# Kernel tuning notes

Hardware: AMD Instinct MI355X
Metric: run time of the kernel (lower is better)

## Reference

```python
import math
import jax, jax.numpy as jnp
import numpy as np

H = 1024          # hidden size
NH = 16           # num attention heads
HD = H // NH      # head dim = 64
MAXPOS = 1024
HYP_W = 0.5


def setup_inputs() -> dict:
    key = jax.random.key(0)
    ks = jax.random.split(key, 9)
    B, S = 4, 1024
    scale = 1.0 / math.sqrt(H)
    return {
        "hidden_states": jax.random.normal(ks[0], (B, S, H), jnp.float32),
        "attention_mask": jnp.zeros((B, 1, 1, S), jnp.float32),
        "hyperbolic_attention_scores": jax.random.normal(ks[1], (B, S, S), jnp.float32),
        "Wq": jax.random.normal(ks[2], (H, H), jnp.float32) * scale,
        "bq": jnp.zeros((H,), jnp.float32),
        "Wk": jax.random.normal(ks[3], (H, H), jnp.float32) * scale,
        "bk": jnp.zeros((H,), jnp.float32),
        "Wv": jax.random.normal(ks[4], (H, H), jnp.float32) * scale,
        "bv": jnp.zeros((H,), jnp.float32),
        "dist_emb": jax.random.normal(ks[5], (2 * MAXPOS - 1, HD), jnp.float32) * 0.02,
    }


def reference(hidden_states, attention_mask, hyperbolic_attention_scores,
              Wq, bq, Wk, bk, Wv, bv, dist_emb):
    B, S, _ = hidden_states.shape

    def split_heads(x):  # [B,S,H] -> [B,NH,S,HD]
        return x.reshape(B, S, NH, HD).transpose(0, 2, 1, 3)

    q = split_heads(hidden_states @ Wq + bq)
    k = split_heads(hidden_states @ Wk + bk)
    v = split_heads(hidden_states @ Wv + bv)

    # raw scores [B,NH,Sq,Sk]
    scores = jnp.einsum("bhqd,bhkd->bhqk", q, k)

    # relative_key_query position bias
    distance = jnp.arange(S)[:, None] - jnp.arange(S)[None, :]  # [Sq,Sk]
    pe = dist_emb[distance + MAXPOS - 1]                        # [Sq,Sk,HD]
    scores = scores + jnp.einsum("bhld,lrd->bhlr", q, pe)
    scores = scores + jnp.einsum("bhrd,lrd->bhlr", k, pe)

    scores = scores / math.sqrt(HD)
    scores = scores + HYP_W * hyperbolic_attention_scores[:, None, :, :]
    scores = scores + attention_mask

    probs = jax.nn.softmax(scores, axis=-1)
    ctx = jnp.einsum("bhqk,bhkd->bhqd", probs, v)  # [B,NH,S,HD]
    ctx = ctx.transpose(0, 2, 1, 3).reshape(B, S, H)
    return ctx
```

## Files before the change

### kernel.cpp

```cpp
#include <hip/hip_runtime.h>
#include <math.h>

#define S_SEQ 1024
#define NHEAD 16
#define HDIM  64
#define BATCH 4

typedef __attribute__((ext_vector_type(8))) short bf16x8;
typedef __attribute__((ext_vector_type(4))) float f32x4;

__device__ __forceinline__ float bf2f(unsigned short h) {
    union { unsigned u; float f; } un; un.u = ((unsigned)h) << 16; return un.f;
}
__device__ __forceinline__ unsigned short f2bf(float x) {
    union { float f; unsigned u; } un; un.f = x;
    unsigned r = un.u + 0x7FFFu + ((un.u >> 16) & 1u);
    return (unsigned short)(r >> 16);
}

#define HS_F4 1048576
#define PE_F4 32752
__global__ __launch_bounds__(256) void conv_kernel(
    const float* __restrict__ hs, const float* __restrict__ de,
    unsigned short* __restrict__ hsb, unsigned short* __restrict__ peb)
{
    int i = blockIdx.x * 256 + threadIdx.x;
    if (i < HS_F4) {
        float4 v = ((const float4*)hs)[i];
        uint2 o;
        o.x = (unsigned)f2bf(v.x) | ((unsigned)f2bf(v.y) << 16);
        o.y = (unsigned)f2bf(v.z) | ((unsigned)f2bf(v.w) << 16);
        *(uint2*)(hsb + 4 * (size_t)i) = o;
    } else if (i < HS_F4 + PE_F4) {
        int j = i - HS_F4;
        float4 v = ((const float4*)de)[j];
        uint2 o;
        o.x = (unsigned)f2bf(v.x) | ((unsigned)f2bf(v.y) << 16);
        o.y = (unsigned)f2bf(v.z) | ((unsigned)f2bf(v.w) << 16);
        *(uint2*)(peb + 4 * (size_t)j) = o;
    }
}

__global__ __launch_bounds__(256) void wtrans_kernel(
    const float* __restrict__ Wq, const float* __restrict__ Wk,
    const float* __restrict__ Wv, unsigned short* __restrict__ wt)
{
    __shared__ float tl[64 * 67];
    const int which = blockIdx.z;
    const float* W = (which == 0) ? Wq : (which == 1) ? Wk : Wv;
    unsigned short* out = wt + (size_t)which * 1024 * 1024;
    const int k0 = blockIdx.x * 64, n0 = blockIdx.y * 64;
    const int t = threadIdx.x;

#pragma unroll
    for (int it = 0; it < 4; ++it) {
        int idx = t + it * 256;
        int kr = idx >> 4;
        int c4 = (idx & 15) << 2;
        float4 v = *(const float4*)(W + (size_t)(k0 + kr) * 1024 + n0 + c4);
        tl[kr * 67 + c4 + 0] = v.x; tl[kr * 67 + c4 + 1] = v.y;
        tl[kr * 67 + c4 + 2] = v.z; tl[kr * 67 + c4 + 3] = v.w;
    }
    __syncthreads();
#pragma unroll
    for (int it = 0; it < 2; ++it) {
        int idx = t + it * 256;
        int nr = idx >> 3;
        int k8 = (idx & 7) << 3;
        unsigned short r[8];
#pragma unroll
        for (int e = 0; e < 8; ++e) r[e] = f2bf(tl[(k8 + e) * 67 + nr]);
        uint4 o;
        o.x = (unsigned)r[0] | ((unsigned)r[1] << 16);
        o.y = (unsigned)r[2] | ((unsigned)r[3] << 16);
        o.z = (unsigned)r[4] | ((unsigned)r[5] << 16);
        o.w = (unsigned)r[6] | ((unsigned)r[7] << 16);
        *(uint4*)(out + (size_t)(n0 + nr) * 1024 + k0 + k8) = o;
    }
}

__global__ __launch_bounds__(256) void qkv_mfma_kernel(
    const unsigned short* __restrict__ hsb, const unsigned short* __restrict__ wt,
    const float* __restrict__ bq, const float* __restrict__ bk,
    const float* __restrict__ bv,
    unsigned short* __restrict__ qo, unsigned short* __restrict__ ko,
    unsigned short* __restrict__ vo)
{
    __shared__ unsigned short As[128 * 40];
    __shared__ unsigned short Bs[128 * 40];

    const int t = threadIdx.x;
    const int lane = t & 63, w = t >> 6;
    const int l16 = lane & 15, quad = lane >> 4;
    const int wm = w >> 1, wn = w & 1;
    const int n0 = blockIdx.x * 128, m0 = blockIdx.y * 128;
    const int which = blockIdx.z;
    const unsigned short* wts = wt + (size_t)which * 1024 * 1024;
    const float* bias = (which == 0) ? bq : (which == 1) ? bk : bv;
    unsigned short* out = (which == 0) ? qo : (which == 1) ? ko : vo;

    f32x4 acc[4][4];
#pragma unroll
    for (int i = 0; i < 4; ++i)
#pragma unroll
        for (int j = 0; j < 4; ++j) acc[i][j] = (f32x4){0.f, 0.f, 0.f, 0.f};

    for (int kk = 0; kk < 1024; kk += 32) {
#pragma unroll
        for (int it = 0; it < 2; ++it) {
            int idx = t + it * 256;
            int row = idx >> 2;
            int c8 = (idx & 3) << 3;
            *(uint4*)&As[row * 40 + c8] =
                *(const uint4*)(hsb + (size_t)(m0 + row) * 1024 + kk + c8);
            *(uint4*)&Bs[row * 40 + c8] =
                *(const uint4*)(wts + (size_t)(n0 + row) * 1024 + kk + c8);
        }
        __syncthreads();
        bf16x8 af[4], bf[4];
#pragma unroll
        for (int i = 0; i < 4; ++i)
            af[i] = *(bf16x8*)&As[(64 * wm + 16 * i + l16) * 40 + quad * 8];
#pragma unroll
        for (int j = 0; j < 4; ++j)
            bf[j] = *(bf16x8*)&Bs[(64 * wn + 16 * j + l16) * 40 + quad * 8];
#pragma unroll
        for (int i = 0; i < 4; ++i)
#pragma unroll
            for (int j = 0; j < 4; ++j)
                acc[i][j] = __builtin_amdgcn_mfma_f32_16x16x32_bf16(
                    af[i], bf[j], acc[i][j], 0, 0, 0);
        __syncthreads();
    }

#pragma unroll
    for (int j = 0; j < 4; ++j) {
        int n = n0 + 64 * wn + 16 * j + l16;
        float bvv = bias[n];
        int hh = n >> 6, hd = n & 63;
#pragma unroll
        for (int i = 0; i < 4; ++i)
#pragma unroll
            for (int r = 0; r < 4; ++r) {
                int m = m0 + 64 * wm + 16 * i + quad * 4 + r;
                int bb = m >> 10, s = m & 1023;
                out[((size_t)(bb * NHEAD + hh) * S_SEQ + s) * HDIM + hd] =
                    f2bf(acc[i][j][r] + bvv);
            }
    }
}

__global__ __launch_bounds__(256, 2) void attn_mfma_kernel(
    const unsigned short* __restrict__ qw, const unsigned short* __restrict__ kw,
    const unsigned short* __restrict__ vw, const unsigned short* __restrict__ peb,
    const float* __restrict__ hyp, const float* __restrict__ mask,
    float* __restrict__ out)
{
    __shared__ unsigned short ks[64 * 72];
    __shared__ unsigned short vsb[64 * 72];
    __shared__ unsigned short pes[128 * 72];
    __shared__ unsigned short QDs[128 * 68];
    __shared__ unsigned short KDs[128 * 68];

    const int t = threadIdx.x;
    const int lane = t & 63, w = t >> 6;
    const int l16 = lane & 15, quad = lane >> 4;
    const int l0 = blockIdx.x * 64;
    const int h = blockIdx.y, b = blockIdx.z;

    const unsigned short* qb = qw + ((size_t)(b * NHEAD + h) * S_SEQ + l0) * HDIM;
    const unsigned short* kb = kw + (size_t)(b * NHEAD + h) * S_SEQ * HDIM;
    const unsigned short* vb = vw + (size_t)(b * NHEAD + h) * S_SEQ * HDIM;
    const float* hypb  = hyp + (size_t)b * S_SEQ * S_SEQ;
    const float* maskb = mask + b * S_SEQ;

    bf16x8 qf[2];
    qf[0] = *(const bf16x8*)(qb + (16 * w + l16) * 64 + quad * 8);
    qf[1] = *(const bf16x8*)(qb + (16 * w + l16) * 64 + 32 + quad * 8);

    if (t < 8) *(uint4*)&pes[127 * 72 + t * 8] = (uint4){0, 0, 0, 0};

    f32x4 accO[4];
#pragma unroll
    for (int j = 0; j < 4; ++j) accO[j] = (f32x4){0.f, 0.f, 0.f, 0.f};
    float m_run[4], lsum[4];
#pragma unroll
    for (int i = 0; i < 4; ++i) { m_run[i] = -INFINITY; lsum[i] = 0.f; }

    for (int kt = 0; kt < 16; ++kt) {
        const int r0 = kt * 64;
        __syncthreads();
#pragma unroll
        for (int it = 0; it < 2; ++it) {
            int idx = t + it * 256;
            int row = idx >> 3, c8 = (idx & 7) << 3;
            *(uint4*)&ks[row * 72 + c8] =
                *(const uint4*)(kb + (size_t)(r0 + row) * 64 + c8);
        }
#pragma unroll
        for (int it = 0; it < 2; ++it) {
            int idx = t + it * 256;
            int vr = idx >> 3, d8 = (idx & 7) << 3;
            uint4 raw = *(const uint4*)(vb + (size_t)(r0 + vr) * 64 + d8);
            const unsigned short* pv = (const unsigned short*)&raw;
            int chunk = (((vr >> 3) ^ (d8 >> 3)) << 3) | (vr & 7);
#pragma unroll
            for (int e = 0; e < 8; ++e) vsb[(d8 + e) * 72 + chunk] = pv[e];
        }
        {
            const size_t pbase = (size_t)(l0 - r0 + 960) * 64;
            for (int idx = t; idx < 1016; idx += 256) {
                int row = idx >> 3, c8 = (idx & 7) << 3;
                *(uint4*)&pes[row * 72 + c8] = *(const uint4*)(peb + pbase + row * 64 + c8);
            }
        }
        __syncthreads();

        bf16x8 kfA[2];
        kfA[0] = *(bf16x8*)&ks[(16 * w + l16) * 72 + quad * 8];
        kfA[1] = *(bf16x8*)&ks[(16 * w + l16) * 72 + 32 + quad * 8];
        f32x4 accS[4];
#pragma unroll
        for (int j = 0; j < 4; ++j) {
            bf16x8 b0 = *(bf16x8*)&ks[(16 * j + l16) * 72 + quad * 8];
            bf16x8 b1 = *(bf16x8*)&ks[(16 * j + l16) * 72 + 32 + quad * 8];
            f32x4 a = (f32x4){0.f, 0.f, 0.f, 0.f};
            a = __builtin_amdgcn_mfma_f32_16x16x32_bf16(qf[0], b0, a, 0, 0, 0);
            a = __builtin_amdgcn_mfma_f32_16x16x32_bf16(qf[1], b1, a, 0, 0, 0);
            accS[j] = a;
        }
#pragma unroll
        for (int jd = 0; jd < 8; ++jd) {
            bf16x8 p0 = *(bf16x8*)&pes[(16 * jd + l16) * 72 + quad * 8];
            bf16x8 p1 = *(bf16x8*)&pes[(16 * jd + l16) * 72 + 32 + quad * 8];
            f32x4 aq = (f32x4){0.f, 0.f, 0.f, 0.f};
            f32x4 ak = (f32x4){0.f, 0.f, 0.f, 0.f};
            aq = __builtin_amdgcn_mfma_f32_16x16x32_bf16(qf[0], p0, aq, 0, 0, 0);
            aq = __builtin_amdgcn_mfma_f32_16x16x32_bf16(qf[1], p1, aq, 0, 0, 0);
            ak = __builtin_amdgcn_mfma_f32_16x16x32_bf16(kfA[0], p0, ak, 0, 0, 0);
            ak = __builtin_amdgcn_mfma_f32_16x16x32_bf16(kfA[1], p1, ak, 0, 0, 0);
            uint2 oq, okk;
            oq.x  = (unsigned)f2bf(aq[0]) | ((unsigned)f2bf(aq[1]) << 16);
            oq.y  = (unsigned)f2bf(aq[2]) | ((unsigned)f2bf(aq[3]) << 16);
            okk.x = (unsigned)f2bf(ak[0]) | ((unsigned)f2bf(ak[1]) << 16);
            okk.y = (unsigned)f2bf(ak[2]) | ((unsigned)f2bf(ak[3]) << 16);
            *(uint2*)&QDs[(16 * jd + l16) * 68 + 16 * w + 4 * quad] = oq;
            *(uint2*)&KDs[(16 * jd + l16) * 68 + 16 * w + 4 * quad] = okk;
        }
        __syncthreads();

        float sc[4][4];
#pragma unroll
        for (int j = 0; j < 4; ++j) {
            int r_loc = 16 * j + l16;
            float mv = maskb[r0 + r_loc];
#pragma unroll
            for (int i = 0; i < 4; ++i) {
                int ll = 16 * w + 4 * quad + i;
                int di = ll - r_loc + 63;
                float qd = bf2f(QDs[di * 68 + ll]);
                float kd = bf2f(KDs[di * 68 + r_loc]);
                float hv = hypb[(size_t)(l0 + ll) * S_SEQ + r0 + r_loc];
                sc[i][j] = (accS[j][i] + qd + kd) * 0.125f + 0.5f * hv + mv;
            }
        }
        float al[4];
#pragma unroll
        for (int i = 0; i < 4; ++i) {
            float mx = fmaxf(fmaxf(sc[i][0], sc[i][1]), fmaxf(sc[i][2], sc[i][3]));
#pragma unroll
            for (int off = 1; off < 16; off <<= 1)
                mx = fmaxf(mx, __shfl_xor(mx, off));
            float m_new = fmaxf(m_run[i], mx);
            al[i] = __expf(m_run[i] - m_new);
            float rs = 0.f;
#pragma unroll
            for (int j = 0; j < 4; ++j) {
                float p = __expf(sc[i][j] - m_new);
                sc[i][j] = p;
                rs += p;
            }
#pragma unroll
            for (int off = 1; off < 16; off <<= 1)
                rs += __shfl_xor(rs, off);
            lsum[i] = lsum[i] * al[i] + rs;
            m_run[i] = m_new;
        }
#pragma unroll
        for (int i = 0; i < 4; ++i)
#pragma unroll
            for (int j = 0; j < 4; ++j)
                pes[(16 * w + 4 * quad + i) * 72 + 16 * j + l16] = f2bf(sc[i][j]);
        __syncthreads();

        bf16x8 pf[2];
        pf[0] = *(bf16x8*)&pes[(16 * w + l16) * 72 + quad * 8];
        pf[1] = *(bf16x8*)&pes[(16 * w + l16) * 72 + 32 + quad * 8];
#pragma unroll
        for (int j = 0; j < 4; ++j) {
            int d = 16 * j + l16;
            int c0 = ((quad ^ (d >> 3)) << 3);
            int c1 = (((4 + quad) ^ (d >> 3)) << 3);
            bf16x8 v0 = *(bf16x8*)&vsb[d * 72 + c0];
            bf16x8 v1 = *(bf16x8*)&vsb[d * 72 + c1];
            f32x4 o = accO[j];
#pragma unroll
            for (int r = 0; r < 4; ++r) o[r] *= al[r];
            o = __builtin_amdgcn_mfma_f32_16x16x32_bf16(pf[0], v0, o, 0, 0, 0);
            o = __builtin_amdgcn_mfma_f32_16x16x32_bf16(pf[1], v1, o, 0, 0, 0);
            accO[j] = o;
        }
    }

#pragma unroll
    for (int j = 0; j < 4; ++j)
#pragma unroll
        for (int i = 0; i < 4; ++i) {
            int ll = 16 * w + 4 * quad + i;
            out[((size_t)b * S_SEQ + l0 + ll) * 1024 + h * 64 + 16 * j + l16] =
                accO[j][i] / lsum[i];
        }
}

extern "C" void kernel_launch(void* const* d_in, const int* in_sizes, int n_in,
                              void* d_out, int out_size, void* d_ws, size_t ws_size,
                              hipStream_t stream) {
    const float* hs   = (const float*)d_in[0];
    const float* mask = (const float*)d_in[1];
    const float* hyp  = (const float*)d_in[2];
    const float* Wq   = (const float*)d_in[3];
    const float* bq   = (const float*)d_in[4];
    const float* Wk   = (const float*)d_in[5];
    const float* bk   = (const float*)d_in[6];
    const float* Wv   = (const float*)d_in[7];
    const float* bv   = (const float*)d_in[8];
    const float* de   = (const float*)d_in[9];

    char* ws = (char*)d_ws;
    unsigned short* qw  = (unsigned short*)(ws);
    unsigned short* kw  = (unsigned short*)(ws + (8u << 20));
    unsigned short* vw  = (unsigned short*)(ws + (16u << 20));
    unsigned short* hsb = (unsigned short*)(ws + (24u << 20));
    unsigned short* wt  = (unsigned short*)(ws + (32u << 20));
    unsigned short* peb = (unsigned short*)(ws + (38u << 20));

    conv_kernel<<<dim3((HS_F4 + PE_F4 + 255) / 256), 256, 0, stream>>>(hs, de, hsb, peb);
    wtrans_kernel<<<dim3(16, 16, 3), 256, 0, stream>>>(Wq, Wk, Wv, wt);
    qkv_mfma_kernel<<<dim3(8, 32, 3), 256, 0, stream>>>(hsb, wt, bq, bk, bv, qw, kw, vw);
    attn_mfma_kernel<<<dim3(16, NHEAD, BATCH), 256, 0, stream>>>(
        qw, kw, vw, peb, hyp, mask, (float*)d_out);
}
```

Baseline: 312.7 us.

## Rework attention with ring-buffered position embeddings, pre-transposed V, and async-LDS QKV loads

The attention kernel now uses 32-key tiles and keeps position-embedding rows in a 96-slot ring buffer, so each tile loads only 32 new rows and computes only the new query-distance products instead of recomputing all of them. The QKV GEMM writes V pre-transposed, which removes the scalar transpose into shared memory inside the attention loop. The GEMM also uses K=64 tiles with XOR-swizzled LDS and global_load_lds direct loads. Occupancy hints rise to 3 blocks per CU. The cost is twice as many tile iterations and barriers, plus more complex slot indexing that could be wrong.

```diff
diff --git a/kernel.cpp b/kernel.cpp
--- a/kernel.cpp
+++ b/kernel.cpp
@@ -16,6 +16,14 @@
     union { float f; unsigned u; } un; un.f = x;
     unsigned r = un.u + 0x7FFFu + ((un.u >> 16) & 1u);
     return (unsigned short)(r >> 16);
+}
+__device__ __forceinline__ unsigned pack2bf(float a, float b) {
+    return (unsigned)f2bf(a) | ((unsigned)f2bf(b) << 16);
+}
+__device__ __forceinline__ void glds16(const unsigned short* g, unsigned short* l) {
+    __builtin_amdgcn_global_load_lds(
+        (const __attribute__((address_space(1))) void*)g,
+        (__attribute__((address_space(3))) void*)l, 16, 0, 0);
 }
 
 #define HS_F4 1048576
@@ -28,15 +36,15 @@
     if (i < HS_F4) {
         float4 v = ((const float4*)hs)[i];
         uint2 o;
-        o.x = (unsigned)f2bf(v.x) | ((unsigned)f2bf(v.y) << 16);
-        o.y = (unsigned)f2bf(v.z) | ((unsigned)f2bf(v.w) << 16);
+        o.x = pack2bf(v.x, v.y);
+        o.y = pack2bf(v.z, v.w);
         *(uint2*)(hsb + 4 * (size_t)i) = o;
     } else if (i < HS_F4 + PE_F4) {
         int j = i - HS_F4;
         float4 v = ((const float4*)de)[j];
         uint2 o;
-        o.x = (unsigned)f2bf(v.x) | ((unsigned)f2bf(v.y) << 16);
-        o.y = (unsigned)f2bf(v.z) | ((unsigned)f2bf(v.w) << 16);
+        o.x = pack2bf(v.x, v.y);
+        o.y = pack2bf(v.z, v.w);
         *(uint2*)(peb + 4 * (size_t)j) = o;
     }
 }
@@ -79,25 +87,25 @@
     }
 }
 
-__global__ __launch_bounds__(256) void qkv_mfma_kernel(
+__global__ __launch_bounds__(256, 3) void qkv_mfma_kernel(
     const unsigned short* __restrict__ hsb, const unsigned short* __restrict__ wt,
     const float* __restrict__ bq, const float* __restrict__ bk,
     const float* __restrict__ bv,
     unsigned short* __restrict__ qo, unsigned short* __restrict__ ko,
     unsigned short* __restrict__ vo)
 {
-    __shared__ unsigned short As[128 * 40];
-    __shared__ unsigned short Bs[128 * 40];
+    __shared__ unsigned short As[128 * 64];
+    __shared__ unsigned short Bs[128 * 64];
 
     const int t = threadIdx.x;
     const int lane = t & 63, w = t >> 6;
     const int l16 = lane & 15, quad = lane >> 4;
     const int wm = w >> 1, wn = w & 1;
+    const int lrow = lane >> 3, cs = lane & 7;
     const int n0 = blockIdx.x * 128, m0 = blockIdx.y * 128;
     const int which = blockIdx.z;
     const unsigned short* wts = wt + (size_t)which * 1024 * 1024;
     const float* bias = (which == 0) ? bq : (which == 1) ? bk : bv;
-    unsigned short* out = (which == 0) ? qo : (which == 1) ? ko : vo;
 
     f32x4 acc[4][4];
 #pragma unroll
@@ -105,31 +113,42 @@
 #pragma unroll
         for (int j = 0; j < 4; ++j) acc[i][j] = (f32x4){0.f, 0.f, 0.f, 0.f};
 
-    for (int kk = 0; kk < 1024; kk += 32) {
-#pragma unroll
-        for (int it = 0; it < 2; ++it) {
-            int idx = t + it * 256;
-            int row = idx >> 2;
-            int c8 = (idx & 3) << 3;
-            *(uint4*)&As[row * 40 + c8] =
-                *(const uint4*)(hsb + (size_t)(m0 + row) * 1024 + kk + c8);
-            *(uint4*)&Bs[row * 40 + c8] =
-                *(const uint4*)(wts + (size_t)(n0 + row) * 1024 + kk + c8);
-        }
-        __syncthreads();
-        bf16x8 af[4], bf[4];
+    for (int kk = 0; kk < 1024; kk += 64) {
+#pragma unroll
+        for (int it = 0; it < 4; ++it) {
+            int mrow = 32 * w + 8 * it + lrow;
+            int kch = cs ^ (mrow & 7);
+            glds16(hsb + (size_t)(m0 + mrow) * 1024 + kk + kch * 8,
+                   &As[(32 * w + 8 * it) * 64]);
+            glds16(wts + (size_t)(n0 + mrow) * 1024 + kk + kch * 8,
+                   &Bs[(32 * w + 8 * it) * 64]);
+        }
+        __syncthreads();
+
+        bf16x8 af[4][2], bf[4][2];
+#pragma unroll
+        for (int i = 0; i < 4; ++i) {
+            int am = 64 * wm + 16 * i + l16;
+            int base = am * 64;
+            af[i][0] = *(bf16x8*)&As[base + ((quad ^ (am & 7)) << 3)];
+            af[i][1] = *(bf16x8*)&As[base + (((quad + 4) ^ (am & 7)) << 3)];
+        }
+#pragma unroll
+        for (int j = 0; j < 4; ++j) {
+            int bn = 64 * wn + 16 * j + l16;
+            int base = bn * 64;
+            bf[j][0] = *(bf16x8*)&Bs[base + ((quad ^ (bn & 7)) << 3)];
+            bf[j][1] = *(bf16x8*)&Bs[base + (((quad + 4) ^ (bn & 7)) << 3)];
+        }
 #pragma unroll
         for (int i = 0; i < 4; ++i)
-            af[i] = *(bf16x8*)&As[(64 * wm + 16 * i + l16) * 40 + quad * 8];
-#pragma unroll
-        for (int j = 0; j < 4; ++j)
-            bf[j] = *(bf16x8*)&Bs[(64 * wn + 16 * j + l16) * 40 + quad * 8];
-#pragma unroll
-        for (int i = 0; i < 4; ++i)
-#pragma unroll
-            for (int j = 0; j < 4; ++j)
+#pragma unroll
+            for (int j = 0; j < 4; ++j) {
                 acc[i][j] = __builtin_amdgcn_mfma_f32_16x16x32_bf16(
-                    af[i], bf[j], acc[i][j], 0, 0, 0);
+                    af[i][0], bf[j][0], acc[i][j], 0, 0, 0);
+                acc[i][j] = __builtin_amdgcn_mfma_f32_16x16x32_bf16(
+                    af[i][1], bf[j][1], acc[i][j], 0, 0, 0);
+            }
         __syncthreads();
     }
 
@@ -139,28 +158,37 @@
         float bvv = bias[n];
         int hh = n >> 6, hd = n & 63;
 #pragma unroll
-        for (int i = 0; i < 4; ++i)
-#pragma unroll
-            for (int r = 0; r < 4; ++r) {
-                int m = m0 + 64 * wm + 16 * i + quad * 4 + r;
-                int bb = m >> 10, s = m & 1023;
-                out[((size_t)(bb * NHEAD + hh) * S_SEQ + s) * HDIM + hd] =
-                    f2bf(acc[i][j][r] + bvv);
+        for (int i = 0; i < 4; ++i) {
+            int mb = m0 + 64 * wm + 16 * i + 4 * quad;
+            int bb = mb >> 10, s = mb & 1023;
+            if (which == 2) {
+                uint2 o;
+                o.x = pack2bf(acc[i][j][0] + bvv, acc[i][j][1] + bvv);
+                o.y = pack2bf(acc[i][j][2] + bvv, acc[i][j][3] + bvv);
+                *(uint2*)(vo + ((size_t)(bb * NHEAD + hh) * HDIM + hd) * S_SEQ + s) = o;
+            } else {
+                unsigned short* out = (which == 0) ? qo : ko;
+#pragma unroll
+                for (int r = 0; r < 4; ++r)
+                    out[((size_t)(bb * NHEAD + hh) * S_SEQ + s + r) * HDIM + hd] =
+                        f2bf(acc[i][j][r] + bvv);
             }
-    }
-}
-
-__global__ __launch_bounds__(256, 2) void attn_mfma_kernel(
+        }
+    }
+}
+
+__global__ __launch_bounds__(256, 3) void attn_mfma_kernel(
     const unsigned short* __restrict__ qw, const unsigned short* __restrict__ kw,
-    const unsigned short* __restrict__ vw, const unsigned short* __restrict__ peb,
+    const unsigned short* __restrict__ vtw, const unsigned short* __restrict__ peb,
     const float* __restrict__ hyp, const float* __restrict__ mask,
     float* __restrict__ out)
 {
-    __shared__ unsigned short ks[64 * 72];
-    __shared__ unsigned short vsb[64 * 72];
-    __shared__ unsigned short pes[128 * 72];
-    __shared__ unsigned short QDs[128 * 68];
-    __shared__ unsigned short KDs[128 * 68];
+    __shared__ unsigned short ks[32 * 72];
+    __shared__ unsigned short vT[64 * 40];
+    __shared__ unsigned short pes[96 * 72];
+    __shared__ unsigned short QDs[96 * 66];
+    __shared__ unsigned short KDs[96 * 38];
+    __shared__ unsigned short ps[64 * 40];
 
     const int t = threadIdx.x;
     const int lane = t & 63, w = t >> 6;
@@ -170,15 +198,37 @@
 
     const unsigned short* qb = qw + ((size_t)(b * NHEAD + h) * S_SEQ + l0) * HDIM;
     const unsigned short* kb = kw + (size_t)(b * NHEAD + h) * S_SEQ * HDIM;
-    const unsigned short* vb = vw + (size_t)(b * NHEAD + h) * S_SEQ * HDIM;
-    const float* hypb  = hyp + (size_t)b * S_SEQ * S_SEQ;
+    const unsigned short* vtb = vtw + (size_t)(b * NHEAD + h) * HDIM * S_SEQ;
+    const float* hypb = hyp + (size_t)b * S_SEQ * S_SEQ;
     const float* maskb = mask + b * S_SEQ;
 
-    bf16x8 qf[2];
-    qf[0] = *(const bf16x8*)(qb + (16 * w + l16) * 64 + quad * 8);
-    qf[1] = *(const bf16x8*)(qb + (16 * w + l16) * 64 + 32 + quad * 8);
-
-    if (t < 8) *(uint4*)&pes[127 * 72 + t * 8] = (uint4){0, 0, 0, 0};
+    const bf16x8 qf0 = *(const bf16x8*)(qb + (16 * w + l16) * 64 + quad * 8);
+    const bf16x8 qf1 = *(const bf16x8*)(qb + (16 * w + l16) * 64 + 32 + quad * 8);
+
+    const int pb0 = l0 + 992;
+
+#pragma unroll
+    for (int it = 0; it < 2; ++it) {
+        int idx = t + it * 256;
+        int row = idx >> 3, c8 = (idx & 7) << 3;
+        int ar = pb0 + 32 + row;
+        int slot = ar % 96;
+        int src = ar > 2046 ? 2046 : ar;
+        *(uint4*)&pes[slot * 72 + c8] = *(const uint4*)(peb + (size_t)src * 64 + c8);
+    }
+    __syncthreads();
+#pragma unroll
+    for (int jd = 0; jd < 4; ++jd) {
+        int slot = (pb0 + 32 + 16 * jd + l16) % 96;
+        bf16x8 p0 = *(bf16x8*)&pes[slot * 72 + quad * 8];
+        bf16x8 p1 = *(bf16x8*)&pes[slot * 72 + 32 + quad * 8];
+        f32x4 aq = (f32x4){0.f, 0.f, 0.f, 0.f};
+        aq = __builtin_amdgcn_mfma_f32_16x16x32_bf16(qf0, p0, aq, 0, 0, 0);
+        aq = __builtin_amdgcn_mfma_f32_16x16x32_bf16(qf1, p1, aq, 0, 0, 0);
+        int ad = slot * 66 + 16 * w + 4 * quad;
+        *(unsigned*)&QDs[ad] = pack2bf(aq[0], aq[1]);
+        *(unsigned*)&QDs[ad + 2] = pack2bf(aq[2], aq[3]);
+    }
 
     f32x4 accO[4];
 #pragma unroll
@@ -187,99 +237,92 @@
 #pragma unroll
     for (int i = 0; i < 4; ++i) { m_run[i] = -INFINITY; lsum[i] = 0.f; }
 
-    for (int kt = 0; kt < 16; ++kt) {
-        const int r0 = kt * 64;
-        __syncthreads();
-#pragma unroll
-        for (int it = 0; it < 2; ++it) {
-            int idx = t + it * 256;
-            int row = idx >> 3, c8 = (idx & 7) << 3;
+    int sb = pb0 % 96;
+
+    for (int kt = 0; kt < 32; ++kt) {
+        const int r0 = 32 * kt;
+        const int pb = pb0 - r0;
+
+        {
+            int row = t >> 3, c8 = (t & 7) << 3;
             *(uint4*)&ks[row * 72 + c8] =
                 *(const uint4*)(kb + (size_t)(r0 + row) * 64 + c8);
-        }
-#pragma unroll
-        for (int it = 0; it < 2; ++it) {
-            int idx = t + it * 256;
-            int vr = idx >> 3, d8 = (idx & 7) << 3;
-            uint4 raw = *(const uint4*)(vb + (size_t)(r0 + vr) * 64 + d8);
-            const unsigned short* pv = (const unsigned short*)&raw;
-            int chunk = (((vr >> 3) ^ (d8 >> 3)) << 3) | (vr & 7);
-#pragma unroll
-            for (int e = 0; e < 8; ++e) vsb[(d8 + e) * 72 + chunk] = pv[e];
-        }
-        {
-            const size_t pbase = (size_t)(l0 - r0 + 960) * 64;
-            for (int idx = t; idx < 1016; idx += 256) {
-                int row = idx >> 3, c8 = (idx & 7) << 3;
-                *(uint4*)&pes[row * 72 + c8] = *(const uint4*)(peb + pbase + row * 64 + c8);
-            }
-        }
-        __syncthreads();
-
-        bf16x8 kfA[2];
-        kfA[0] = *(bf16x8*)&ks[(16 * w + l16) * 72 + quad * 8];
-        kfA[1] = *(bf16x8*)&ks[(16 * w + l16) * 72 + 32 + quad * 8];
-        f32x4 accS[4];
-#pragma unroll
-        for (int j = 0; j < 4; ++j) {
+            int d = t >> 2, rc = (t & 3) << 3;
+            *(uint4*)&vT[d * 40 + rc] =
+                *(const uint4*)(vtb + (size_t)d * 1024 + r0 + rc);
+            int slot = sb + row; if (slot >= 96) slot -= 96;
+            *(uint4*)&pes[slot * 72 + c8] =
+                *(const uint4*)(peb + (size_t)(pb + row) * 64 + c8);
+        }
+        __syncthreads();
+
+        bf16x8 kfA0 = *(bf16x8*)&ks[(16 * (w & 1) + l16) * 72 + quad * 8];
+        bf16x8 kfA1 = *(bf16x8*)&ks[(16 * (w & 1) + l16) * 72 + 32 + quad * 8];
+        f32x4 accS[2];
+#pragma unroll
+        for (int j = 0; j < 2; ++j) {
             bf16x8 b0 = *(bf16x8*)&ks[(16 * j + l16) * 72 + quad * 8];
             bf16x8 b1 = *(bf16x8*)&ks[(16 * j + l16) * 72 + 32 + quad * 8];
             f32x4 a = (f32x4){0.f, 0.f, 0.f, 0.f};
-            a = __builtin_amdgcn_mfma_f32_16x16x32_bf16(qf[0], b0, a, 0, 0, 0);
-            a = __builtin_amdgcn_mfma_f32_16x16x32_bf16(qf[1], b1, a, 0, 0, 0);
+            a = __builtin_amdgcn_mfma_f32_16x16x32_bf16(qf0, b0, a, 0, 0, 0);
+            a = __builtin_amdgcn_mfma_f32_16x16x32_bf16(qf1, b1, a, 0, 0, 0);
             accS[j] = a;
         }
 #pragma unroll
-        for (int jd = 0; jd < 8; ++jd) {
-            bf16x8 p0 = *(bf16x8*)&pes[(16 * jd + l16) * 72 + quad * 8];
-            bf16x8 p1 = *(bf16x8*)&pes[(16 * jd + l16) * 72 + 32 + quad * 8];
+        for (int jd = 0; jd < 2; ++jd) {
+            int slot = sb + 16 * jd + l16; if (slot >= 96) slot -= 96;
+            bf16x8 p0 = *(bf16x8*)&pes[slot * 72 + quad * 8];
+            bf16x8 p1 = *(bf16x8*)&pes[slot * 72 + 32 + quad * 8];
             f32x4 aq = (f32x4){0.f, 0.f, 0.f, 0.f};
+            aq = __builtin_amdgcn_mfma_f32_16x16x32_bf16(qf0, p0, aq, 0, 0, 0);
+            aq = __builtin_amdgcn_mfma_f32_16x16x32_bf16(qf1, p1, aq, 0, 0, 0);
+            int ad = slot * 66 + 16 * w + 4 * quad;
+            *(unsigned*)&QDs[ad] = pack2bf(aq[0], aq[1]);
+            *(unsigned*)&QDs[ad + 2] = pack2bf(aq[2], aq[3]);
+        }
+#pragma unroll
+        for (int jk = 0; jk < 3; ++jk) {
+            int dd = 48 * (w >> 1) + 16 * jk + l16;
+            int slot = sb + dd; if (slot >= 96) slot -= 96;
+            bf16x8 p0 = *(bf16x8*)&pes[slot * 72 + quad * 8];
+            bf16x8 p1 = *(bf16x8*)&pes[slot * 72 + 32 + quad * 8];
             f32x4 ak = (f32x4){0.f, 0.f, 0.f, 0.f};
-            aq = __builtin_amdgcn_mfma_f32_16x16x32_bf16(qf[0], p0, aq, 0, 0, 0);
-            aq = __builtin_amdgcn_mfma_f32_16x16x32_bf16(qf[1], p1, aq, 0, 0, 0);
-            ak = __builtin_amdgcn_mfma_f32_16x16x32_bf16(kfA[0], p0, ak, 0, 0, 0);
-            ak = __builtin_amdgcn_mfma_f32_16x16x32_bf16(kfA[1], p1, ak, 0, 0, 0);
-            uint2 oq, okk;
-            oq.x  = (unsigned)f2bf(aq[0]) | ((unsigned)f2bf(aq[1]) << 16);
-            oq.y  = (unsigned)f2bf(aq[2]) | ((unsigned)f2bf(aq[3]) << 16);
-            okk.x = (unsigned)f2bf(ak[0]) | ((unsigned)f2bf(ak[1]) << 16);
-            okk.y = (unsigned)f2bf(ak[2]) | ((unsigned)f2bf(ak[3]) << 16);
-            *(uint2*)&QDs[(16 * jd + l16) * 68 + 16 * w + 4 * quad] = oq;
-            *(uint2*)&KDs[(16 * jd + l16) * 68 + 16 * w + 4 * quad] = okk;
-        }
-        __syncthreads();
-
-        float sc[4][4];
-#pragma unroll
-        for (int j = 0; j < 4; ++j) {
+            ak = __builtin_amdgcn_mfma_f32_16x16x32_bf16(kfA0, p0, ak, 0, 0, 0);
+            ak = __builtin_amdgcn_mfma_f32_16x16x32_bf16(kfA1, p1, ak, 0, 0, 0);
+            int ad = dd * 38 + 16 * (w & 1) + 4 * quad;
+            *(unsigned*)&KDs[ad] = pack2bf(ak[0], ak[1]);
+            *(unsigned*)&KDs[ad + 2] = pack2bf(ak[2], ak[3]);
+        }
+        __syncthreads();
+
+        float sc[4][2], al[4];
+#pragma unroll
+        for (int j = 0; j < 2; ++j) {
             int r_loc = 16 * j + l16;
             float mv = maskb[r0 + r_loc];
 #pragma unroll
             for (int i = 0; i < 4; ++i) {
                 int ll = 16 * w + 4 * quad + i;
-                int di = ll - r_loc + 63;
-                float qd = bf2f(QDs[di * 68 + ll]);
-                float kd = bf2f(KDs[di * 68 + r_loc]);
-                float hv = hypb[(size_t)(l0 + ll) * S_SEQ + r0 + r_loc];
+                int di = ll - r_loc + 31;
+                int sl = sb + di; if (sl >= 96) sl -= 96;
+                float qd = bf2f(QDs[sl * 66 + ll]);
+                float kd = bf2f(KDs[di * 38 + r_loc]);
+                float hv = hypb[(size_t)(l0 + ll) * 1024 + r0 + r_loc];
                 sc[i][j] = (accS[j][i] + qd + kd) * 0.125f + 0.5f * hv + mv;
             }
         }
-        float al[4];
-#pragma unroll
-        for (int i = 0; i < 4; ++i) {
-            float mx = fmaxf(fmaxf(sc[i][0], sc[i][1]), fmaxf(sc[i][2], sc[i][3]));
+#pragma unroll
+        for (int i = 0; i < 4; ++i) {
+            float mx = fmaxf(sc[i][0], sc[i][1]);
 #pragma unroll
             for (int off = 1; off < 16; off <<= 1)
                 mx = fmaxf(mx, __shfl_xor(mx, off));
             float m_new = fmaxf(m_run[i], mx);
             al[i] = __expf(m_run[i] - m_new);
-            float rs = 0.f;
-#pragma unroll
-            for (int j = 0; j < 4; ++j) {
-                float p = __expf(sc[i][j] - m_new);
-                sc[i][j] = p;
-                rs += p;
-            }
+            float p0 = __expf(sc[i][0] - m_new);
+            float p1 = __expf(sc[i][1] - m_new);
+            sc[i][0] = p0; sc[i][1] = p1;
+            float rs = p0 + p1;
 #pragma unroll
             for (int off = 1; off < 16; off <<= 1)
                 rs += __shfl_xor(rs, off);
@@ -287,38 +330,33 @@
             m_run[i] = m_new;
         }
 #pragma unroll
-        for (int i = 0; i < 4; ++i)
-#pragma unroll
-            for (int j = 0; j < 4; ++j)
-                pes[(16 * w + 4 * quad + i) * 72 + 16 * j + l16] = f2bf(sc[i][j]);
-        __syncthreads();
-
-        bf16x8 pf[2];
-        pf[0] = *(bf16x8*)&pes[(16 * w + l16) * 72 + quad * 8];
-        pf[1] = *(bf16x8*)&pes[(16 * w + l16) * 72 + 32 + quad * 8];
-#pragma unroll
-        for (int j = 0; j < 4; ++j) {
-            int d = 16 * j + l16;
-            int c0 = ((quad ^ (d >> 3)) << 3);
-            int c1 = (((4 + quad) ^ (d >> 3)) << 3);
-            bf16x8 v0 = *(bf16x8*)&vsb[d * 72 + c0];
-            bf16x8 v1 = *(bf16x8*)&vsb[d * 72 + c1];
-            f32x4 o = accO[j];
+        for (int i = 0; i < 4; ++i) {
+            int ll = 16 * w + 4 * quad + i;
+            ps[ll * 40 + l16] = f2bf(sc[i][0]);
+            ps[ll * 40 + 16 + l16] = f2bf(sc[i][1]);
+        }
+
+        bf16x8 pf = *(bf16x8*)&ps[(16 * w + l16) * 40 + quad * 8];
+#pragma unroll
+        for (int jf = 0; jf < 4; ++jf) {
+            bf16x8 vv = *(bf16x8*)&vT[(16 * jf + l16) * 40 + quad * 8];
+            f32x4 o = accO[jf];
 #pragma unroll
             for (int r = 0; r < 4; ++r) o[r] *= al[r];
-            o = __builtin_amdgcn_mfma_f32_16x16x32_bf16(pf[0], v0, o, 0, 0, 0);
-            o = __builtin_amdgcn_mfma_f32_16x16x32_bf16(pf[1], v1, o, 0, 0, 0);
-            accO[j] = o;
-        }
-    }
-
-#pragma unroll
-    for (int j = 0; j < 4; ++j)
+            o = __builtin_amdgcn_mfma_f32_16x16x32_bf16(pf, vv, o, 0, 0, 0);
+            accO[jf] = o;
+        }
+        sb -= 32; if (sb < 0) sb += 96;
+        __syncthreads();
+    }
+
+#pragma unroll
+    for (int jf = 0; jf < 4; ++jf)
 #pragma unroll
         for (int i = 0; i < 4; ++i) {
             int ll = 16 * w + 4 * quad + i;
-            out[((size_t)b * S_SEQ + l0 + ll) * 1024 + h * 64 + 16 * j + l16] =
-                accO[j][i] / lsum[i];
+            out[((size_t)b * S_SEQ + l0 + ll) * 1024 + h * 64 + 16 * jf + l16] =
+                accO[jf][i] / lsum[i];
         }
 }
 
@@ -339,14 +377,14 @@
     char* ws = (char*)d_ws;
     unsigned short* qw  = (unsigned short*)(ws);
     unsigned short* kw  = (unsigned short*)(ws + (8u << 20));
-    unsigned short* vw  = (unsigned short*)(ws + (16u << 20));
+    unsigned short* vtw = (unsigned short*)(ws + (16u << 20));
     unsigned short* hsb = (unsigned short*)(ws + (24u << 20));
     unsigned short* wt  = (unsigned short*)(ws + (32u << 20));
     unsigned short* peb = (unsigned short*)(ws + (38u << 20));
 
     conv_kernel<<<dim3((HS_F4 + PE_F4 + 255) / 256), 256, 0, stream>>>(hs, de, hsb, peb);
     wtrans_kernel<<<dim3(16, 16, 3), 256, 0, stream>>>(Wq, Wk, Wv, wt);
-    qkv_mfma_kernel<<<dim3(8, 32, 3), 256, 0, stream>>>(hsb, wt, bq, bk, bv, qw, kw, vw);
+    qkv_mfma_kernel<<<dim3(8, 32, 3), 256, 0, stream>>>(hsb, wt, bq, bk, bv, qw, kw, vtw);
     attn_mfma_kernel<<<dim3(16, NHEAD, BATCH), 256, 0, stream>>>(
-        qw, kw, vw, peb, hyp, mask, (float*)d_out);
-}
+        qw, kw, vtw, peb, hyp, mask, (float*)d_out);
+}
```

Result: faster. 286.9 us (-8.3%).
